# Kernel tuning notes

Measured on AMD Instinct MI355X. Metric: run time of the kernel, lower is better.

The kernel has to match this reference:

```python
import jax, jax.numpy as jnp
import numpy as np

N = 100000
H = 8      # heads
C = 8      # out channels per head
NEG_SLOPE = 0.2
EPS = 1e-16


def setup_inputs() -> dict:
    key = jax.random.key(0)
    k1, k2, k3, k4, k5, k6 = jax.random.split(key, 6)
    x = jax.random.normal(k1, (N, 128), dtype=jnp.float32)
    edge_index = jax.random.randint(k2, (2, 1600000), 0, N, dtype=jnp.int64)
    W = jax.random.normal(k3, (128, H * C), dtype=jnp.float32) * (1.0 / np.sqrt(128))
    att_src = jax.random.normal(k4, (H, C), dtype=jnp.float32)
    att_dst = jax.random.normal(k5, (H, C), dtype=jnp.float32)
    bias = jax.random.normal(k6, (H * C,), dtype=jnp.float32) * 0.01
    return {"x": x, "edge_index": edge_index, "W": W,
            "att_src": att_src, "att_dst": att_dst, "bias": bias}


def _gat_forward(x, edge_index, W, att_src, att_dst, bias):
    # add self loops (PyG GATConv default add_self_loops=True)
    loop = jnp.arange(N, dtype=edge_index.dtype)
    src = jnp.concatenate([edge_index[0], loop])
    dst = jnp.concatenate([edge_index[1], loop])

    h = (x @ W).reshape(N, H, C)                       # [N,H,C]
    a_src = jnp.sum(h * att_src, axis=-1)              # [N,H]
    a_dst = jnp.sum(h * att_dst, axis=-1)              # [N,H]

    e = a_src[src] + a_dst[dst]                        # [E,H]
    e = jnp.where(e > 0, e, NEG_SLOPE * e)             # leaky_relu(0.2)

    # segment softmax over edges grouped by destination node
    m = jax.ops.segment_max(e, dst, num_segments=N)    # [N,H]
    m = jnp.where(jnp.isfinite(m), m, 0.0)
    ex = jnp.exp(e - m[dst])                           # [E,H]
    denom = jax.ops.segment_sum(ex, dst, num_segments=N)
    alpha = ex / (denom[dst] + EPS)                    # [E,H]

    msg = alpha[:, :, None] * h[src]                   # [E,H,C]
    out = jax.ops.segment_sum(msg, dst, num_segments=N)  # [N,H,C]
    out = out.reshape(N, H * C) + bias
    return jax.nn.relu(out)


def reference(x, edge_index, W, att_src, att_dst, bias):
    return _gat_forward(x, edge_index, W, att_src, att_dst, bias)
```

## Files before the change

kernel.cpp:

```cpp
#include <hip/hip_runtime.h>
#include <hip/hip_bf16.h>

#define NNODES 100000
#define NH 8
#define OUTD 64
#define FDIM 128
#define NEG_SLOPE 0.2f
#define NBUCK ((NNODES + 255) / 256)
#define MAXB 5376
#define CH 8192
#define ROWS_PB 128
#define NFB ((NNODES + ROWS_PB - 1) / ROWS_PB)
#define HSTRIDE 68

typedef __attribute__((ext_vector_type(8))) short bf16x8;
typedef __attribute__((ext_vector_type(4))) float f32x4;

static __device__ __forceinline__ unsigned short f2bf(float f) {
    __hip_bfloat16 b = __float2bfloat16(f);
    return *(unsigned short*)&b;
}

__global__ __launch_bounds__(256) void k_featbin(
    const float* __restrict__ x, const float* __restrict__ W,
    const float* __restrict__ att_s, const float* __restrict__ att_d,
    const int* __restrict__ ei, int E,
    __hip_bfloat16* __restrict__ h, float* __restrict__ asrc,
    float* __restrict__ adst, int* __restrict__ gCur,
    unsigned int* __restrict__ gSorted)
{
    int tid = threadIdx.x;

    if (blockIdx.x >= NFB) {
        __shared__ int cnt[NBUCK];
        __shared__ int base[NBUCK];
        int tot = E + NNODES;
        int e0 = (blockIdx.x - NFB) * CH;
        int e1 = e0 + CH; if (e1 > tot) e1 = tot;

        for (int i = tid; i < NBUCK; i += 256) cnt[i] = 0;
        __syncthreads();

        for (int i = e0 + tid; i < e1; i += 256) {
            int d = (i < E) ? ei[E + i] : (i - E);
            atomicAdd(&cnt[d >> 8], 1);
        }
        __syncthreads();

        for (int i = tid; i < NBUCK; i += 256) {
            int c = cnt[i];
            base[i] = (c > 0) ? atomicAdd(&gCur[i], c) : 0;
            cnt[i] = 0;
        }
        __syncthreads();

        for (int i = e0 + tid; i < e1; i += 256) {
            int s, d;
            if (i < E) { s = ei[i]; d = ei[E + i]; }
            else       { s = d = i - E; }
            int b = d >> 8;
            int p = base[b] + atomicAdd(&cnt[b], 1);
            if (p < MAXB)
                gSorted[(size_t)b * MAXB + p] =
                    ((unsigned int)(d & 255) << 17) | (unsigned int)s;
        }
        return;
    }

    __shared__ unsigned short swt[OUTD * FDIM];
    __shared__ unsigned short shb[4 * 16 * HSTRIDE];
    __shared__ float slgs[4 * 128];
    __shared__ float slgd[4 * 128];

    for (int i = tid; i < OUTD * 16; i += 256) {
        int col = i & 63, chunk = i >> 6;
        unsigned short tmp[8];
#pragma unroll
        for (int j = 0; j < 8; ++j)
            tmp[j] = f2bf(W[(chunk * 8 + j) * OUTD + col]);
        int chs = chunk ^ (col & 15);
        *(bf16x8*)&swt[col * FDIM + chs * 8] = *(bf16x8*)tmp;
    }
    __syncthreads();

    int w = tid >> 6, l = tid & 63;
    int l4 = l & 15, g = l >> 4;
    int row0 = blockIdx.x * ROWS_PB;

    bf16x8 bfrag[16];
#pragma unroll
    for (int n = 0; n < 4; ++n)
#pragma unroll
        for (int kk = 0; kk < 4; ++kk) {
            int col = n * 16 + l4;
            int chs = (kk * 4 + g) ^ l4;
            bfrag[n * 4 + kk] = *(const bf16x8*)&swt[col * FDIM + chs * 8];
        }

    float as_r[4], ad_r[4];
#pragma unroll
    for (int n = 0; n < 4; ++n) {
        as_r[n] = att_s[n * 16 + l4];
        ad_r[n] = att_d[n * 16 + l4];
    }

    unsigned short* myh = &shb[w * 16 * HSTRIDE];
    float* myls = &slgs[w * 128];
    float* myld = &slgd[w * 128];

#pragma unroll
    for (int rt = 0; rt < 2; ++rt) {
        int lbase = w * 32 + rt * 16;
        int grow_a = row0 + lbase + l4;
        bool va = grow_a < NNODES;

        f32x4 xa[8];
        const float* xp = x + (size_t)grow_a * FDIM + g * 8;
        if (va) {
#pragma unroll
            for (int kk = 0; kk < 4; ++kk) {
                xa[2 * kk]     = *(const f32x4*)(xp + kk * 32);
                xa[2 * kk + 1] = *(const f32x4*)(xp + kk * 32 + 4);
            }
        } else {
#pragma unroll
            for (int i = 0; i < 8; ++i) xa[i] = (f32x4){0.f, 0.f, 0.f, 0.f};
        }
        bf16x8 af[4];
#pragma unroll
        for (int kk = 0; kk < 4; ++kk)
#pragma unroll
            for (int j = 0; j < 4; ++j) {
                af[kk][j]     = (short)f2bf(xa[2 * kk][j]);
                af[kk][4 + j] = (short)f2bf(xa[2 * kk + 1][j]);
            }

        f32x4 acc[4];
#pragma unroll
        for (int n = 0; n < 4; ++n) acc[n] = (f32x4){0.f, 0.f, 0.f, 0.f};
#pragma unroll
        for (int kk = 0; kk < 4; ++kk)
#pragma unroll
            for (int n = 0; n < 4; ++n)
                acc[n] = __builtin_amdgcn_mfma_f32_16x16x32_bf16(
                    af[kk], bfrag[n * 4 + kk], acc[n], 0, 0, 0);

#pragma unroll
        for (int n = 0; n < 4; ++n)
#pragma unroll
            for (int r = 0; r < 4; ++r)
                myh[(g * 4 + r) * HSTRIDE + n * 16 + l4] = f2bf(acc[n][r]);

#pragma unroll
        for (int n = 0; n < 4; ++n)
#pragma unroll
            for (int r = 0; r < 4; ++r) {
                float vs = acc[n][r] * as_r[n];
                float vd = acc[n][r] * ad_r[n];
                vs += __shfl_xor(vs, 1); vs += __shfl_xor(vs, 2); vs += __shfl_xor(vs, 4);
                vd += __shfl_xor(vd, 1); vd += __shfl_xor(vd, 2); vd += __shfl_xor(vd, 4);
                if ((l & 7) == 0) {
                    int row = g * 4 + r, hd = 2 * n + (l4 >> 3);
                    myls[row * 8 + hd] = vs;
                    myld[row * 8 + hd] = vd;
                }
            }

#pragma unroll
        for (int i = 0; i < 2; ++i) {
            int c = i * 64 + l;
            int row = c >> 3, ch = c & 7;
            int grow = row0 + lbase + row;
            if (grow < NNODES) {
                bf16x8 v = *(const bf16x8*)&myh[row * HSTRIDE + ch * 8];
                *(bf16x8*)&h[(size_t)grow * OUTD + ch * 8] = v;
            }
        }
#pragma unroll
        for (int i = 0; i < 2; ++i) {
            int c = i * 64 + l;
            int row = c >> 3, hd = c & 7;
            int grow = row0 + lbase + row;
            if (grow < NNODES) {
                asrc[grow * NH + hd] = myls[row * 8 + hd];
                adst[grow * NH + hd] = myld[row * 8 + hd];
            }
        }
    }
}

__global__ __launch_bounds__(256) void k_csr(
    const int* __restrict__ gCur, unsigned int* __restrict__ gSorted,
    int2* __restrict__ rows)
{
    __shared__ unsigned int ent[MAXB];
    __shared__ int cnt[256], cur[256];
    __shared__ int wsum[4];
    int b = blockIdx.x;
    int n = gCur[b]; if (n > MAXB) n = MAXB;
    size_t gbase = (size_t)b * MAXB;
    int tid = threadIdx.x;

    for (int i = tid; i < n; i += 256) ent[i] = gSorted[gbase + i];
    cnt[tid] = 0;
    __syncthreads();

    for (int i = tid; i < n; i += 256)
        atomicAdd(&cnt[ent[i] >> 17], 1);
    __syncthreads();

    int v = cnt[tid];
    int lane = tid & 63, wid = tid >> 6;
    int acc = v;
#pragma unroll
    for (int off = 1; off < 64; off <<= 1) {
        int t = __shfl_up(acc, off);
        if (lane >= off) acc += t;
    }
    if (lane == 63) wsum[wid] = acc;
    __syncthreads();
    int woff = 0;
#pragma unroll
    for (int i = 0; i < 4; ++i) woff += (i < wid) ? wsum[i] : 0;
    int ex = acc + woff - v;

    int node = (b << 8) + tid;
    if (node < NNODES)
        rows[node] = make_int2((int)gbase + ex, (int)gbase + ex + v);
    cur[tid] = ex;
    __syncthreads();

    for (int i = tid; i < n; i += 256) {
        unsigned int p = ent[i];
        int pos = atomicAdd(&cur[p >> 17], 1);
        gSorted[gbase + pos] = p & 0x1FFFFu;
    }
}

__global__ __launch_bounds__(256) void k_gather(
    const int2* __restrict__ rows, const unsigned int* __restrict__ esrc,
    const __hip_bfloat16* __restrict__ h, const float* __restrict__ asrc,
    const float* __restrict__ adst, const float* __restrict__ bias,
    float* __restrict__ out)
{
    int node = (blockIdx.x * 256 + threadIdx.x) >> 6;
    if (node >= NNODES) return;
    int lane = threadIdx.x & 63;
    int slot = lane >> 4;
    int li   = lane & 15;
    int hh   = li >> 1;

    float adh = adst[(unsigned)(node * NH + hh)];
    int2 se = rows[node];
    const uint2* hu = (const uint2*)h;

    float n0 = 0.f, n1 = 0.f, n2 = 0.f, n3 = 0.f, den = 0.f;

    for (int base = se.x; base < se.y; base += 64) {
        int cnt = se.y - base; if (cnt > 64) cnt = 64;
        int sj = (lane < cnt) ? (int)esrc[base + lane] : 0;

        int k = 0;
        for (; k + 8 <= cnt; k += 8) {
            int sA = __shfl(sj, k + slot);
            int sB = __shfl(sj, k + 4 + slot);
            float aA = asrc[(unsigned)(sA * NH + hh)];
            float aB = asrc[(unsigned)(sB * NH + hh)];
            uint2 wA = hu[(unsigned)(sA * 16 + li)];
            uint2 wB = hu[(unsigned)(sB * 16 + li)];
            float eA = aA + adh; eA = fmaxf(eA, NEG_SLOPE * eA); eA = __expf(eA);
            float eB = aB + adh; eB = fmaxf(eB, NEG_SLOPE * eB); eB = __expf(eB);
            den += eA; den += eB;
            union { unsigned u; float f; } t;
            t.u = wA.x << 16;         n0 = fmaf(eA, t.f, n0);
            t.u = wA.x & 0xffff0000u; n1 = fmaf(eA, t.f, n1);
            t.u = wA.y << 16;         n2 = fmaf(eA, t.f, n2);
            t.u = wA.y & 0xffff0000u; n3 = fmaf(eA, t.f, n3);
            t.u = wB.x << 16;         n0 = fmaf(eB, t.f, n0);
            t.u = wB.x & 0xffff0000u; n1 = fmaf(eB, t.f, n1);
            t.u = wB.y << 16;         n2 = fmaf(eB, t.f, n2);
            t.u = wB.y & 0xffff0000u; n3 = fmaf(eB, t.f, n3);
        }
        for (; k < cnt; k += 4) {
            int s2 = __shfl(sj, k + slot);
            bool valid = (k + slot) < cnt;
            float a = asrc[(unsigned)(s2 * NH + hh)];
            uint2 w = hu[(unsigned)(s2 * 16 + li)];
            float e = a + adh; e = fmaxf(e, NEG_SLOPE * e);
            float ex = valid ? __expf(e) : 0.f;
            den += ex;
            union { unsigned u; float f; } t;
            t.u = w.x << 16;         n0 = fmaf(ex, t.f, n0);
            t.u = w.x & 0xffff0000u; n1 = fmaf(ex, t.f, n1);
            t.u = w.y << 16;         n2 = fmaf(ex, t.f, n2);
            t.u = w.y & 0xffff0000u; n3 = fmaf(ex, t.f, n3);
        }
    }

    n0 += __shfl_xor(n0, 16); n0 += __shfl_xor(n0, 32);
    n1 += __shfl_xor(n1, 16); n1 += __shfl_xor(n1, 32);
    n2 += __shfl_xor(n2, 16); n2 += __shfl_xor(n2, 32);
    n3 += __shfl_xor(n3, 16); n3 += __shfl_xor(n3, 32);
    den += __shfl_xor(den, 16); den += __shfl_xor(den, 32);

    if (slot == 0) {
        float inv = 1.f / (den + 1e-16f);
        int ch = li * 4;
        float4 v;
        v.x = fmaxf(n0 * inv + bias[ch + 0], 0.f);
        v.y = fmaxf(n1 * inv + bias[ch + 1], 0.f);
        v.z = fmaxf(n2 * inv + bias[ch + 2], 0.f);
        v.w = fmaxf(n3 * inv + bias[ch + 3], 0.f);
        *(float4*)&out[(unsigned)(node * OUTD + ch)] = v;
    }
}

extern "C" void kernel_launch(void* const* d_in, const int* in_sizes, int n_in,
                              void* d_out, int out_size, void* d_ws, size_t ws_size,
                              hipStream_t stream)
{
    const float* x     = (const float*)d_in[0];
    const int*   ei    = (const int*)  d_in[1];
    const float* W     = (const float*)d_in[2];
    const float* att_s = (const float*)d_in[3];
    const float* att_d = (const float*)d_in[4];
    const float* bias  = (const float*)d_in[5];
    float* out = (float*)d_out;
    int E = in_sizes[1] / 2;
    int tot = E + NNODES;

    __hip_bfloat16* h = (__hip_bfloat16*)d_ws;
    float* asrc   = (float*)(h + (size_t)NNODES * OUTD);
    float* adst   = asrc + (size_t)NNODES * NH;
    int2*  rows   = (int2*)(adst + (size_t)NNODES * NH);
    int*   gCur   = (int*)(rows + NNODES);
    unsigned int* gSorted = (unsigned int*)(gCur + 512);

    hipMemsetAsync(gCur, 0, 512 * sizeof(int), stream);

    int nbin = (tot + CH - 1) / CH;
    k_featbin<<<NFB + nbin, 256, 0, stream>>>(x, W, att_s, att_d, ei, E,
                                              h, asrc, adst, gCur, gSorted);
    k_csr<<<NBUCK, 256, 0, stream>>>(gCur, gSorted, rows);
    k_gather<<<(NNODES * 64 + 255) / 256, 256, 0, stream>>>(
        rows, gSorted, h, asrc, adst, bias, out);
}
```

Measured before the change: 115.0 us.

## Interleave feature and binning blocks, prebuild swizzled bf16 W, register-cache edges

Adds a small pre-kernel that converts W to a swizzled bf16 image once, so each feature block copies it into LDS with vector loads instead of converting strided fp32 itself. Feature and edge-binning blocks are now interleaved in blockIdx order so memory-bound binning overlaps compute-bound GEMM work across the GPU. The binning chunk size drops to 2048 edges, and each thread keeps its 8 edges in registers, avoiding a second read of edge_index. The cost is one extra kernel launch and more binning blocks issuing global atomics on gCur.

```diff
diff --git a/kernel.cpp b/kernel.cpp
--- a/kernel.cpp
+++ b/kernel.cpp
@@ -8,61 +8,86 @@
 #define NEG_SLOPE 0.2f
 #define NBUCK ((NNODES + 255) / 256)
 #define MAXB 5376
-#define CH 8192
+#define CH 2048
 #define ROWS_PB 128
 #define NFB ((NNODES + ROWS_PB - 1) / ROWS_PB)
 #define HSTRIDE 68
 
 typedef __attribute__((ext_vector_type(8))) short bf16x8;
 typedef __attribute__((ext_vector_type(4))) float f32x4;
+typedef __attribute__((ext_vector_type(4))) unsigned int u32x4;
 
 static __device__ __forceinline__ unsigned short f2bf(float f) {
     __hip_bfloat16 b = __float2bfloat16(f);
     return *(unsigned short*)&b;
 }
 
+__global__ void k_wprep(const float* __restrict__ W, unsigned short* __restrict__ wimg)
+{
+    int i = blockIdx.x * 256 + threadIdx.x;
+    if (i >= FDIM * OUTD) return;
+    int k = i >> 6, col = i & 63;
+    int chs = (k >> 3) ^ (col & 15);
+    wimg[col * FDIM + chs * 8 + (k & 7)] = f2bf(W[i]);
+}
+
 __global__ __launch_bounds__(256) void k_featbin(
-    const float* __restrict__ x, const float* __restrict__ W,
+    const float* __restrict__ x, const unsigned short* __restrict__ wimg,
     const float* __restrict__ att_s, const float* __restrict__ att_d,
-    const int* __restrict__ ei, int E,
+    const int* __restrict__ ei, int E, int nbin,
     __hip_bfloat16* __restrict__ h, float* __restrict__ asrc,
     float* __restrict__ adst, int* __restrict__ gCur,
     unsigned int* __restrict__ gSorted)
 {
     int tid = threadIdx.x;
 
-    if (blockIdx.x >= NFB) {
+    int b = blockIdx.x;
+    int nPair = (NFB < nbin) ? NFB : nbin;
+    bool isbin; int idx;
+    if (b < 2 * nPair) { isbin = (b & 1); idx = b >> 1; }
+    else { int r = b - 2 * nPair; isbin = (NFB <= nbin); idx = nPair + r; }
+
+    if (isbin) {
         __shared__ int cnt[NBUCK];
-        __shared__ int base[NBUCK];
+        __shared__ int basearr[NBUCK];
         int tot = E + NNODES;
-        int e0 = (blockIdx.x - NFB) * CH;
+        int e0 = idx * CH;
         int e1 = e0 + CH; if (e1 > tot) e1 = tot;
 
         for (int i = tid; i < NBUCK; i += 256) cnt[i] = 0;
         __syncthreads();
 
-        for (int i = e0 + tid; i < e1; i += 256) {
-            int d = (i < E) ? ei[E + i] : (i - E);
-            atomicAdd(&cnt[d >> 8], 1);
+        int ss[8], dd[8];
+#pragma unroll
+        for (int i = 0; i < 8; ++i) {
+            int e = e0 + i * 256 + tid;
+            int s = 0, d = -1;
+            if (e < e1) {
+                if (e < E) { s = ei[e]; d = ei[E + e]; }
+                else       { s = d = e - E; }
+                atomicAdd(&cnt[d >> 8], 1);
+            }
+            ss[i] = s; dd[i] = d;
         }
         __syncthreads();
 
         for (int i = tid; i < NBUCK; i += 256) {
             int c = cnt[i];
-            base[i] = (c > 0) ? atomicAdd(&gCur[i], c) : 0;
+            basearr[i] = (c > 0) ? atomicAdd(&gCur[i], c) : 0;
             cnt[i] = 0;
         }
         __syncthreads();
 
-        for (int i = e0 + tid; i < e1; i += 256) {
-            int s, d;
-            if (i < E) { s = ei[i]; d = ei[E + i]; }
-            else       { s = d = i - E; }
-            int b = d >> 8;
-            int p = base[b] + atomicAdd(&cnt[b], 1);
-            if (p < MAXB)
-                gSorted[(size_t)b * MAXB + p] =
-                    ((unsigned int)(d & 255) << 17) | (unsigned int)s;
+#pragma unroll
+        for (int i = 0; i < 8; ++i) {
+            int d = dd[i];
+            if (d >= 0) {
+                int bk = d >> 8;
+                int p = basearr[bk] + atomicAdd(&cnt[bk], 1);
+                if (p < MAXB)
+                    gSorted[(size_t)bk * MAXB + p] =
+                        ((unsigned int)(d & 255) << 17) | (unsigned int)ss[i];
+            }
         }
         return;
     }
@@ -72,20 +97,16 @@
     __shared__ float slgs[4 * 128];
     __shared__ float slgd[4 * 128];
 
-    for (int i = tid; i < OUTD * 16; i += 256) {
-        int col = i & 63, chunk = i >> 6;
-        unsigned short tmp[8];
-#pragma unroll
-        for (int j = 0; j < 8; ++j)
-            tmp[j] = f2bf(W[(chunk * 8 + j) * OUTD + col]);
-        int chs = chunk ^ (col & 15);
-        *(bf16x8*)&swt[col * FDIM + chs * 8] = *(bf16x8*)tmp;
+    {
+        const u32x4* src = (const u32x4*)wimg;
+        u32x4* dst = (u32x4*)swt;
+        for (int i = tid; i < (OUTD * FDIM) / 8; i += 256) dst[i] = src[i];
     }
     __syncthreads();
 
     int w = tid >> 6, l = tid & 63;
     int l4 = l & 15, g = l >> 4;
-    int row0 = blockIdx.x * ROWS_PB;
+    int row0 = idx * ROWS_PB;
 
     bf16x8 bfrag[16];
 #pragma unroll
@@ -328,6 +349,7 @@
     float* out = (float*)d_out;
     int E = in_sizes[1] / 2;
     int tot = E + NNODES;
+    int nbin = (tot + CH - 1) / CH;
 
     __hip_bfloat16* h = (__hip_bfloat16*)d_ws;
     float* asrc   = (float*)(h + (size_t)NNODES * OUTD);
@@ -335,11 +357,12 @@
     int2*  rows   = (int2*)(adst + (size_t)NNODES * NH);
     int*   gCur   = (int*)(rows + NNODES);
     unsigned int* gSorted = (unsigned int*)(gCur + 512);
+    unsigned short* wimg  = (unsigned short*)(gSorted + (size_t)NBUCK * MAXB);
 
     hipMemsetAsync(gCur, 0, 512 * sizeof(int), stream);
 
-    int nbin = (tot + CH - 1) / CH;
-    k_featbin<<<NFB + nbin, 256, 0, stream>>>(x, W, att_s, att_d, ei, E,
+    k_wprep<<<(FDIM * OUTD + 255) / 256, 256, 0, stream>>>(W, wimg);
+    k_featbin<<<NFB + nbin, 256, 0, stream>>>(x, wimg, att_s, att_d, ei, E, nbin,
                                               h, asrc, adst, gCur, gSorted);
     k_csr<<<NBUCK, 256, 0, stream>>>(gCur, gSorted, rows);
     k_gather<<<(NNODES * 64 + 255) / 256, 256, 0, stream>>>(
```

Measured after the change: 113.0 us. About the same (-1.7%).
